# Kernel tuning notes

Hardware: AMD Instinct MI355X
Metric: run time of the kernel (lower is better)

Reference implementation:

```python
import jax, jax.numpy as jnp
import numpy as np

EMBED_DIM = 1024
WINDOW = 256
NUM_HEADS = 16
HEAD_DIM = EMBED_DIM // NUM_HEADS
SCALE = HEAD_DIM ** (-0.5)


def setup_inputs() -> dict:
    key = jax.random.key(0)
    ks = jax.random.split(key, 9)
    B, S, E = 4, 4096, EMBED_DIM
    std = E ** (-0.5)
    x = jax.random.normal(ks[0], (B, S, E), dtype=jnp.float32)
    Wq = jax.random.normal(ks[1], (E, E), dtype=jnp.float32) * std
    Wk = jax.random.normal(ks[2], (E, E), dtype=jnp.float32) * std
    Wv = jax.random.normal(ks[3], (E, E), dtype=jnp.float32) * std
    Wo = jax.random.normal(ks[4], (E, E), dtype=jnp.float32) * std
    bq = jax.random.normal(ks[5], (E,), dtype=jnp.float32) * 0.01
    bk = jax.random.normal(ks[6], (E,), dtype=jnp.float32) * 0.01
    bv = jax.random.normal(ks[7], (E,), dtype=jnp.float32) * 0.01
    bo = jax.random.normal(ks[8], (E,), dtype=jnp.float32) * 0.01
    return {"x": x, "Wq": Wq, "bq": bq, "Wk": Wk, "bk": bk,
            "Wv": Wv, "bv": bv, "Wo": Wo, "bo": bo}


def reference(x, Wq, bq, Wk, bk, Wv, bv, Wo, bo):
    B, S, E = x.shape
    W = WINDOW
    nw = S // W  # seq_len chosen divisible by window_size
    # projections (torch Linear: x @ W.T + b); no head split in the original
    q = x @ Wq.T + bq
    k = x @ Wk.T + bk
    v = x @ Wv.T + bv
    # split into non-overlapping windows: [B, nw, W, E]
    qw = q.reshape(B, nw, W, E)
    kw = k.reshape(B, nw, W, E)
    vw = v.reshape(B, nw, W, E)
    scores = jnp.einsum('bnqe,bnke->bnqk', qw, kw) * SCALE  # [B, nw, W, W]
    causal = jnp.tril(jnp.ones((W, W), dtype=bool))
    scores = jnp.where(causal, scores, -jnp.inf)
    attn = jax.nn.softmax(scores, axis=-1)
    out = jnp.einsum('bnqk,bnke->bnqe', attn, vw).reshape(B, S, E)
    out = out @ Wo.T + bo
    return out + x
```

## Files before the change

kernel.cpp:

```cpp
#include <hip/hip_runtime.h>
#include <hip/hip_bf16.h>


typedef unsigned short u16;
typedef __attribute__((ext_vector_type(8))) short short8;
typedef __attribute__((ext_vector_type(4))) float f32x4;

__device__ __forceinline__ u16 f2bf(float f) {
    __hip_bfloat16 h = __float2bfloat16(f);
    return __builtin_bit_cast(u16, h);
}

__global__ void cast_x(const float* __restrict__ x, u16* __restrict__ xb, u16* __restrict__ xt) {
    __shared__ float lt[64][65];
    const int t = threadIdx.x;
    const int e0 = blockIdx.x * 64, i0 = blockIdx.y * 64;
    const int tr = t >> 3, tc = (t & 7) * 8;
#pragma unroll
    for (int p = 0; p < 2; ++p) {
        int r = p * 32 + tr;
        const float* s = x + (size_t)(i0 + r) * 1024 + e0 + tc;
        float4 a = *(const float4*)s, b = *(const float4*)(s + 4);
        short8 o;
        o[0] = (short)f2bf(a.x); o[1] = (short)f2bf(a.y); o[2] = (short)f2bf(a.z); o[3] = (short)f2bf(a.w);
        o[4] = (short)f2bf(b.x); o[5] = (short)f2bf(b.y); o[6] = (short)f2bf(b.z); o[7] = (short)f2bf(b.w);
        *(short8*)(xb + (size_t)(i0 + r) * 1024 + e0 + tc) = o;
        lt[r][tc + 0] = a.x; lt[r][tc + 1] = a.y; lt[r][tc + 2] = a.z; lt[r][tc + 3] = a.w;
        lt[r][tc + 4] = b.x; lt[r][tc + 5] = b.y; lt[r][tc + 6] = b.z; lt[r][tc + 7] = b.w;
    }
    __syncthreads();
#pragma unroll
    for (int p = 0; p < 2; ++p) {
        int r = p * 32 + tr;
        short8 o;
#pragma unroll
        for (int j = 0; j < 8; ++j) o[j] = (short)f2bf(lt[tc + j][r]);
        *(short8*)(xt + (size_t)(e0 + r) * 16384 + i0 + tc) = o;
    }
}

__global__ void wcast(const float* __restrict__ Wq, const float* __restrict__ Wk,
                      const float* __restrict__ Wv, const float* __restrict__ Wo,
                      u16* __restrict__ WqT, u16* __restrict__ WkT,
                      u16* __restrict__ WvT, u16* __restrict__ Wob)
{
    __shared__ float lt[64][65];
    const int which = blockIdx.x >> 8;
    const int bid = blockIdx.x & 255;
    const int c0 = (bid & 15) * 64, r0 = (bid >> 4) * 64;
    const int t = threadIdx.x;
    const int tr = t >> 3, tc = (t & 7) * 8;
    const float* src = which == 0 ? Wq : which == 1 ? Wk : which == 2 ? Wv : Wo;
    if (which == 3) {
#pragma unroll
        for (int p = 0; p < 2; ++p) {
            int r = p * 32 + tr;
            const float* s = src + (size_t)(r0 + r) * 1024 + c0 + tc;
            float4 a = *(const float4*)s, b = *(const float4*)(s + 4);
            short8 o;
            o[0] = (short)f2bf(a.x); o[1] = (short)f2bf(a.y); o[2] = (short)f2bf(a.z); o[3] = (short)f2bf(a.w);
            o[4] = (short)f2bf(b.x); o[5] = (short)f2bf(b.y); o[6] = (short)f2bf(b.z); o[7] = (short)f2bf(b.w);
            *(short8*)(Wob + (size_t)(r0 + r) * 1024 + c0 + tc) = o;
        }
        return;
    }
    u16* dst = which == 0 ? WqT : which == 1 ? WkT : WvT;
#pragma unroll
    for (int p = 0; p < 2; ++p) {
        int r = p * 32 + tr;
        const float* s = src + (size_t)(r0 + r) * 1024 + c0 + tc;
        float4 a = *(const float4*)s, b = *(const float4*)(s + 4);
        lt[r][tc + 0] = a.x; lt[r][tc + 1] = a.y; lt[r][tc + 2] = a.z; lt[r][tc + 3] = a.w;
        lt[r][tc + 4] = b.x; lt[r][tc + 5] = b.y; lt[r][tc + 6] = b.z; lt[r][tc + 7] = b.w;
    }
    __syncthreads();
#pragma unroll
    for (int p = 0; p < 2; ++p) {
        int r = p * 32 + tr;
        short8 o;
#pragma unroll
        for (int j = 0; j < 8; ++j) o[j] = (short)f2bf(lt[tc + j][r]);
        *(short8*)(dst + (size_t)(c0 + r) * 1024 + r0 + tc) = o;
    }
}

__global__ void ub2(const float* __restrict__ Wk, const float* __restrict__ bq,
                    const float* __restrict__ Wo, const float* __restrict__ bv,
                    const float* __restrict__ bo, float* __restrict__ u, float* __restrict__ b2)
{
    const int t = threadIdx.x, bid = blockIdx.x;
    if (bid < 4) {
        int b = bid * 256 + t;
        float acc = 0.f;
        for (int o = 0; o < 1024; ++o) acc += Wk[(size_t)o * 1024 + b] * bq[o];
        u[b] = acc;
    } else {
        int n = (bid - 4) * 16 + (t >> 4);
        int l = t & 15;
        float acc = 0.f;
        for (int m = l; m < 1024; m += 16) acc += Wo[(size_t)n * 1024 + m] * bv[m];
#pragma unroll
        for (int s = 1; s < 16; s <<= 1) acc += __shfl_xor(acc, s, 64);
        if (l == 0) b2[n] = acc + bo[n];
    }
}

__global__ __launch_bounds__(256, 4) void gemm_small_dual(
    const u16* __restrict__ HA, const u16* __restrict__ HB, u16* __restrict__ HC,
    const u16* __restrict__ WA, const u16* __restrict__ WB, u16* __restrict__ WC)
{
    __shared__ __align__(16) u16 At[64 * 64], Bt[64 * 64];
    const bool sec = blockIdx.x >= 256;
    const u16* A = sec ? WA : HA;
    const u16* B = sec ? WB : HB;
    u16* C = sec ? WC : HC;
    const int bid = blockIdx.x & 255;
    const int m0 = (bid >> 4) * 64, n0 = (bid & 15) * 64;
    const int t = threadIdx.x, lane = t & 63, w = t >> 6;
    const int l15 = lane & 15, lk = lane >> 4;

    f32x4 acc[4];
#pragma unroll
    for (int m = 0; m < 4; ++m) acc[m] = (f32x4){0.f, 0.f, 0.f, 0.f};

    for (int k0 = 0; k0 < 1024; k0 += 64) {
        __syncthreads();
#pragma unroll
        for (int p = 0; p < 2; ++p) {
            int e = p * 2048 + t * 8;
            int row = e >> 6, col = e & 63;
            short8 va = *(const short8*)(A + (size_t)(m0 + row) * 1024 + k0 + col);
            *(short8*)((char*)At + row * 128 + ((col * 2) ^ ((row & 7) << 4))) = va;
            short8 vb = *(const short8*)(B + (size_t)(n0 + row) * 1024 + k0 + col);
            *(short8*)((char*)Bt + row * 128 + ((col * 2) ^ ((row & 7) << 4))) = vb;
        }
        __syncthreads();
#pragma unroll
        for (int ks = 0; ks < 2; ++ks) {
            int bc = ks * 64 + lk * 16;
            int brow = w * 16 + l15;
            short8 bfr = *(const short8*)((char*)Bt + brow * 128 + (bc ^ ((brow & 7) << 4)));
#pragma unroll
            for (int m = 0; m < 4; ++m) {
                int arow = m * 16 + l15;
                short8 af = *(const short8*)((char*)At + arow * 128 + (bc ^ ((arow & 7) << 4)));
                acc[m] = __builtin_amdgcn_mfma_f32_16x16x32_bf16(af, bfr, acc[m], 0, 0, 0);
            }
        }
    }
#pragma unroll
    for (int m = 0; m < 4; ++m)
#pragma unroll
        for (int r = 0; r < 4; ++r) {
            int row = m0 + m * 16 + lk * 4 + r;
            int col = n0 + w * 16 + l15;
            C[(size_t)row * 1024 + col] = f2bf(acc[m][r]);
        }
}

template <int EPI>
__global__ __launch_bounds__(256, 2) void gemm_bt(
    const u16* __restrict__ A, const u16* __restrict__ B,
    int M, int N, int K,
    const float* __restrict__ bias0,
    u16* __restrict__ Cb, float* __restrict__ Cf, const float* __restrict__ resid)
{
    __shared__ __align__(16) u16 At[128 * 64];
    __shared__ __align__(16) u16 Bt[128 * 64];
    const int t = threadIdx.x;
    const int lane = t & 63;
    const int wid = t >> 6;
    const int wm = wid >> 1, wn = wid & 1;
    const int l15 = lane & 15, lk = lane >> 4;

    const int bid = blockIdx.y * gridDim.x + blockIdx.x;
    const int nwg = gridDim.x * gridDim.y;
    const int cpx = nwg >> 3;
    const int swz = (bid & 7) * cpx + (bid >> 3);
    const int tn = swz & 7;
    const int tm = swz >> 3;
    const int m0 = tm * 128, n0 = tn * 128;

    const int srow = (t * 8) >> 6, scol = (t * 8) & 63;

    f32x4 acc[4][4];
#pragma unroll
    for (int m = 0; m < 4; ++m)
#pragma unroll
        for (int n = 0; n < 4; ++n)
            acc[m][n] = (f32x4){0.f, 0.f, 0.f, 0.f};

    short8 pva[4], pvb[4];
#pragma unroll
    for (int p = 0; p < 4; ++p) {
        pva[p] = *(const short8*)(A + (size_t)(m0 + p * 32 + srow) * K + scol);
        pvb[p] = *(const short8*)(B + (size_t)(n0 + p * 32 + srow) * K + scol);
    }

    for (int k0 = 0; k0 < K; k0 += 64) {
        __syncthreads();
#pragma unroll
        for (int p = 0; p < 4; ++p) {
            int row = p * 32 + srow;
            *(short8*)((char*)At + row * 128 + ((scol * 2) ^ ((row & 7) << 4))) = pva[p];
            *(short8*)((char*)Bt + row * 128 + ((scol * 2) ^ ((row & 7) << 4))) = pvb[p];
        }
        __syncthreads();
        if (k0 + 64 < K) {
#pragma unroll
            for (int p = 0; p < 4; ++p) {
                pva[p] = *(const short8*)(A + (size_t)(m0 + p * 32 + srow) * K + k0 + 64 + scol);
                pvb[p] = *(const short8*)(B + (size_t)(n0 + p * 32 + srow) * K + k0 + 64 + scol);
            }
        }
#pragma unroll
        for (int ks = 0; ks < 2; ++ks) {
            const int bc = ks * 64 + lk * 16;
            short8 af[4], bfr[4];
#pragma unroll
            for (int m = 0; m < 4; ++m) {
                int row = wm * 64 + m * 16 + l15;
                af[m] = *(const short8*)((char*)At + row * 128 + (bc ^ ((row & 7) << 4)));
            }
#pragma unroll
            for (int n = 0; n < 4; ++n) {
                int row = wn * 64 + n * 16 + l15;
                bfr[n] = *(const short8*)((char*)Bt + row * 128 + (bc ^ ((row & 7) << 4)));
            }
#pragma unroll
            for (int m = 0; m < 4; ++m)
#pragma unroll
                for (int n = 0; n < 4; ++n)
                    acc[m][n] = __builtin_amdgcn_mfma_f32_16x16x32_bf16(af[m], bfr[n], acc[m][n], 0, 0, 0);
        }
    }

#pragma unroll
    for (int m = 0; m < 4; ++m) {
#pragma unroll
        for (int n = 0; n < 4; ++n) {
            int col = n0 + wn * 64 + n * 16 + l15;
            float bv = bias0[col];
#pragma unroll
            for (int r = 0; r < 4; ++r) {
                int row = m0 + wm * 64 + m * 16 + lk * 4 + r;
                float v = acc[m][n][r] + bv;
                if (EPI == 0)
                    Cb[(size_t)row * N + col] = f2bf(v);
                else
                    Cf[(size_t)row * N + col] = v + resid[(size_t)row * N + col];
            }
        }
    }
}

__global__ __launch_bounds__(256, 2) void attn_win(
    const u16* __restrict__ y, const u16* __restrict__ xb,
    const u16* __restrict__ xt, u16* __restrict__ z)
{
    __shared__ __align__(16) char smem[75776];
    u16* Qt = (u16*)smem;
    u16* Kt = (u16*)(smem + 8192);
    u16* Vl = (u16*)smem;
    u16* P  = (u16*)(smem + 40960);
    float* rmax = (float*)(smem + 73728);
    float* rsum = (float*)(smem + 74752);

    const int t = threadIdx.x;
    const int lane = t & 63, wv = t >> 6;
    const int l15 = lane & 15, lk = lane >> 4;
    const int bid = blockIdx.x;
    const int swz = (bid & 7) * 32 + (bid >> 3);
    const int win = swz >> 2, qc = swz & 3;
    const size_t qrow0 = (size_t)win * 256 + qc * 64;
    const size_t krow0 = (size_t)win * 256;

    f32x4 acc[4][4];
#pragma unroll
    for (int m = 0; m < 4; ++m)
#pragma unroll
        for (int n = 0; n < 4; ++n)
            acc[m][n] = (f32x4){0.f, 0.f, 0.f, 0.f};

    for (int e0 = 0; e0 < 1024; e0 += 64) {
        __syncthreads();
#pragma unroll
        for (int p = 0; p < 2; ++p) {
            int e = p * 2048 + t * 8;
            int row = e >> 6, col = e & 63;
            short8 v = *(const short8*)(y + (qrow0 + row) * 1024 + e0 + col);
            *(short8*)((char*)Qt + row * 128 + ((col * 2) ^ ((row & 7) << 4))) = v;
        }
#pragma unroll
        for (int p = 0; p < 8; ++p) {
            int e = p * 2048 + t * 8;
            int row = e >> 6, col = e & 63;
            short8 v = *(const short8*)(xb + (krow0 + row) * 1024 + e0 + col);
            *(short8*)((char*)Kt + row * 128 + ((col * 2) ^ ((row & 7) << 4))) = v;
        }
        __syncthreads();
#pragma unroll
        for (int ks = 0; ks < 2; ++ks) {
            const int bc = ks * 64 + lk * 16;
            short8 af[4], bfr[4];
#pragma unroll
            for (int m = 0; m < 4; ++m) {
                int row = m * 16 + l15;
                af[m] = *(const short8*)((char*)Qt + row * 128 + (bc ^ ((row & 7) << 4)));
            }
#pragma unroll
            for (int n = 0; n < 4; ++n) {
                int row = wv * 64 + n * 16 + l15;
                bfr[n] = *(const short8*)((char*)Kt + row * 128 + (bc ^ ((row & 7) << 4)));
            }
            __builtin_amdgcn_s_setprio(1);
#pragma unroll
            for (int m = 0; m < 4; ++m)
#pragma unroll
                for (int n = 0; n < 4; ++n)
                    acc[m][n] = __builtin_amdgcn_mfma_f32_16x16x32_bf16(af[m], bfr[n], acc[m][n], 0, 0, 0);
            __builtin_amdgcn_s_setprio(0);
        }
    }

#pragma unroll
    for (int m = 0; m < 4; ++m)
#pragma unroll
        for (int n = 0; n < 4; ++n) {
            int col = wv * 64 + n * 16 + l15;
#pragma unroll
            for (int r = 0; r < 4; ++r) {
                int qpos = qc * 64 + m * 16 + lk * 4 + r;
                float v = acc[m][n][r] * 0.125f;
                acc[m][n][r] = (col <= qpos) ? v : -1e30f;
            }
        }
#pragma unroll
    for (int m = 0; m < 4; ++m)
#pragma unroll
        for (int r = 0; r < 4; ++r) {
            float tmx = fmaxf(fmaxf(acc[m][0][r], acc[m][1][r]), fmaxf(acc[m][2][r], acc[m][3][r]));
            tmx = fmaxf(tmx, __shfl_xor(tmx, 1));
            tmx = fmaxf(tmx, __shfl_xor(tmx, 2));
            tmx = fmaxf(tmx, __shfl_xor(tmx, 4));
            tmx = fmaxf(tmx, __shfl_xor(tmx, 8));
            if (l15 == 0) rmax[(m * 16 + lk * 4 + r) * 4 + wv] = tmx;
        }
    __syncthreads();
#pragma unroll
    for (int m = 0; m < 4; ++m)
#pragma unroll
        for (int r = 0; r < 4; ++r) {
            int row = m * 16 + lk * 4 + r;
            float m4 = fmaxf(fmaxf(rmax[row * 4], rmax[row * 4 + 1]),
                             fmaxf(rmax[row * 4 + 2], rmax[row * 4 + 3]));
            float s = 0.f;
#pragma unroll
            for (int n = 0; n < 4; ++n) {
                float e = __expf(acc[m][n][r] - m4);
                acc[m][n][r] = e;
                s += e;
            }
            s += __shfl_xor(s, 1);
            s += __shfl_xor(s, 2);
            s += __shfl_xor(s, 4);
            s += __shfl_xor(s, 8);
            if (l15 == 0) rsum[row * 4 + wv] = s;
        }
    __syncthreads();
#pragma unroll
    for (int m = 0; m < 4; ++m)
#pragma unroll
        for (int r = 0; r < 4; ++r) {
            int row = m * 16 + lk * 4 + r;
            float inv = 1.f / (rsum[row * 4] + rsum[row * 4 + 1] + rsum[row * 4 + 2] + rsum[row * 4 + 3]);
#pragma unroll
            for (int n = 0; n < 4; ++n) {
                int col = wv * 64 + n * 16 + l15;
                *(u16*)((char*)P + row * 512 + ((col * 2) ^ ((row & 7) << 4))) = f2bf(acc[m][n][r] * inv);
            }
        }

    for (int n0 = 0; n0 < 1024; n0 += 64) {
        __syncthreads();
#pragma unroll
        for (int p = 0; p < 8; ++p) {
            int e = p * 2048 + t * 8;
            int row = e >> 8, col = e & 255;
            short8 v = *(const short8*)(xt + (size_t)(n0 + row) * 16384 + win * 256 + col);
            *(short8*)((char*)Vl + row * 512 + ((col * 2) ^ ((row & 7) << 4))) = v;
        }
        __syncthreads();
        f32x4 acc2[4];
#pragma unroll
        for (int m = 0; m < 4; ++m) acc2[m] = (f32x4){0.f, 0.f, 0.f, 0.f};
#pragma unroll
        for (int ks = 0; ks < 8; ++ks) {
            const int bc = ks * 64 + lk * 16;
            short8 af[4];
#pragma unroll
            for (int m = 0; m < 4; ++m) {
                int row = m * 16 + l15;
                af[m] = *(const short8*)((char*)P + row * 512 + (bc ^ ((row & 7) << 4)));
            }
            int vrow = wv * 16 + l15;
            short8 bfr = *(const short8*)((char*)Vl + vrow * 512 + (bc ^ ((vrow & 7) << 4)));
            __builtin_amdgcn_s_setprio(1);
#pragma unroll
            for (int m = 0; m < 4; ++m)
                acc2[m] = __builtin_amdgcn_mfma_f32_16x16x32_bf16(af[m], bfr, acc2[m], 0, 0, 0);
            __builtin_amdgcn_s_setprio(0);
        }
#pragma unroll
        for (int m = 0; m < 4; ++m) {
#pragma unroll
            for (int r = 0; r < 4; ++r) {
                int row = m * 16 + lk * 4 + r;
                int col = n0 + wv * 16 + l15;
                z[(qrow0 + row) * 1024 + col] = f2bf(acc2[m][r]);
            }
        }
    }
}

extern "C" void kernel_launch(void* const* d_in, const int* in_sizes, int n_in,
                              void* d_out, int out_size, void* d_ws, size_t ws_size,
                              hipStream_t stream) {
    const float* x  = (const float*)d_in[0];
    const float* Wq = (const float*)d_in[1];
    const float* bq = (const float*)d_in[2];
    const float* Wk = (const float*)d_in[3];
    const float* Wv = (const float*)d_in[5];
    const float* bv = (const float*)d_in[6];
    const float* Wo = (const float*)d_in[7];
    const float* bo = (const float*)d_in[8];
    float* out = (float*)d_out;

    char* ws = (char*)d_ws;
    u16* xb  = (u16*)(ws);
    u16* xt  = (u16*)(ws + 33554432);
    u16* yb  = (u16*)(ws + 67108864);
    u16* zb  = (u16*)(ws + 100663296);
    u16* WqT = (u16*)(ws + 134217728);
    u16* WkT = (u16*)(ws + 136314880);
    u16* WvT = (u16*)(ws + 138412032);
    u16* Wob = (u16*)(ws + 140509184);
    u16* Hb  = (u16*)(ws + 142606336);
    u16* W2b = (u16*)(ws + 144703488);
    float* u_  = (float*)(ws + 146800640);
    float* b2_ = (float*)(ws + 146804736);

    cast_x<<<dim3(16, 256), 256, 0, stream>>>(x, xb, xt);
    wcast<<<1024, 256, 0, stream>>>(Wq, Wk, Wv, Wo, WqT, WkT, WvT, Wob);
    ub2<<<68, 256, 0, stream>>>(Wk, bq, Wo, bv, bo, u_, b2_);
    gemm_small_dual<<<512, 256, 0, stream>>>(WkT, WqT, Hb, Wob, WvT, W2b);
    gemm_bt<0><<<dim3(8, 128), 256, 0, stream>>>(xb, Hb, 16384, 1024, 1024, u_, yb, nullptr, nullptr);
    attn_win<<<256, 256, 0, stream>>>(yb, xb, xt, zb);
    gemm_bt<1><<<dim3(8, 128), 256, 0, stream>>>(zb, W2b, 16384, 1024, 1024, b2_, nullptr, out, x);
}
```

Measured before the change: 223.4 us.

## Widen GEMM blocks to 8 waves and halve attention query tile

```diff
diff --git a/kernel.cpp b/kernel.cpp
--- a/kernel.cpp
+++ b/kernel.cpp
@@ -159,7 +159,7 @@
 }
 
 template <int EPI>
-__global__ __launch_bounds__(256, 2) void gemm_bt(
+__global__ __launch_bounds__(512, 4) void gemm_bt(
     const u16* __restrict__ A, const u16* __restrict__ B,
     int M, int N, int K,
     const float* __restrict__ bias0,
@@ -169,8 +169,8 @@
     __shared__ __align__(16) u16 Bt[128 * 64];
     const int t = threadIdx.x;
     const int lane = t & 63;
-    const int wid = t >> 6;
-    const int wm = wid >> 1, wn = wid & 1;
+    const int w = t >> 6;
+    const int wm = w >> 2, wn = w & 3;
     const int l15 = lane & 15, lk = lane >> 4;
 
     const int bid = blockIdx.y * gridDim.x + blockIdx.x;
@@ -181,70 +181,58 @@
     const int tm = swz >> 3;
     const int m0 = tm * 128, n0 = tn * 128;
 
-    const int srow = (t * 8) >> 6, scol = (t * 8) & 63;
-
-    f32x4 acc[4][4];
-#pragma unroll
-    for (int m = 0; m < 4; ++m)
-#pragma unroll
-        for (int n = 0; n < 4; ++n)
-            acc[m][n] = (f32x4){0.f, 0.f, 0.f, 0.f};
-
-    short8 pva[4], pvb[4];
-#pragma unroll
-    for (int p = 0; p < 4; ++p) {
-        pva[p] = *(const short8*)(A + (size_t)(m0 + p * 32 + srow) * K + scol);
-        pvb[p] = *(const short8*)(B + (size_t)(n0 + p * 32 + srow) * K + scol);
-    }
+    const int srow = t >> 3, scol = (t & 7) * 8;
+
+    f32x4 acc[4][2];
+#pragma unroll
+    for (int mf = 0; mf < 4; ++mf)
+#pragma unroll
+        for (int nf = 0; nf < 2; ++nf)
+            acc[mf][nf] = (f32x4){0.f, 0.f, 0.f, 0.f};
 
     for (int k0 = 0; k0 < K; k0 += 64) {
         __syncthreads();
 #pragma unroll
-        for (int p = 0; p < 4; ++p) {
-            int row = p * 32 + srow;
-            *(short8*)((char*)At + row * 128 + ((scol * 2) ^ ((row & 7) << 4))) = pva[p];
-            *(short8*)((char*)Bt + row * 128 + ((scol * 2) ^ ((row & 7) << 4))) = pvb[p];
-        }
-        __syncthreads();
-        if (k0 + 64 < K) {
-#pragma unroll
-            for (int p = 0; p < 4; ++p) {
-                pva[p] = *(const short8*)(A + (size_t)(m0 + p * 32 + srow) * K + k0 + 64 + scol);
-                pvb[p] = *(const short8*)(B + (size_t)(n0 + p * 32 + srow) * K + k0 + 64 + scol);
-            }
-        }
+        for (int p = 0; p < 2; ++p) {
+            int row = p * 64 + srow;
+            short8 va = *(const short8*)(A + (size_t)(m0 + row) * K + k0 + scol);
+            *(short8*)((char*)At + row * 128 + ((scol * 2) ^ ((row & 7) << 4))) = va;
+            short8 vb = *(const short8*)(B + (size_t)(n0 + row) * K + k0 + scol);
+            *(short8*)((char*)Bt + row * 128 + ((scol * 2) ^ ((row & 7) << 4))) = vb;
+        }
+        __syncthreads();
 #pragma unroll
         for (int ks = 0; ks < 2; ++ks) {
             const int bc = ks * 64 + lk * 16;
-            short8 af[4], bfr[4];
-#pragma unroll
-            for (int m = 0; m < 4; ++m) {
-                int row = wm * 64 + m * 16 + l15;
-                af[m] = *(const short8*)((char*)At + row * 128 + (bc ^ ((row & 7) << 4)));
-            }
-#pragma unroll
-            for (int n = 0; n < 4; ++n) {
-                int row = wn * 64 + n * 16 + l15;
-                bfr[n] = *(const short8*)((char*)Bt + row * 128 + (bc ^ ((row & 7) << 4)));
-            }
-#pragma unroll
-            for (int m = 0; m < 4; ++m)
-#pragma unroll
-                for (int n = 0; n < 4; ++n)
-                    acc[m][n] = __builtin_amdgcn_mfma_f32_16x16x32_bf16(af[m], bfr[n], acc[m][n], 0, 0, 0);
-        }
-    }
-
-#pragma unroll
-    for (int m = 0; m < 4; ++m) {
-#pragma unroll
-        for (int n = 0; n < 4; ++n) {
-            int col = n0 + wn * 64 + n * 16 + l15;
+            short8 af[4], bfr[2];
+#pragma unroll
+            for (int mf = 0; mf < 4; ++mf) {
+                int row = wm * 64 + mf * 16 + l15;
+                af[mf] = *(const short8*)((char*)At + row * 128 + (bc ^ ((row & 7) << 4)));
+            }
+#pragma unroll
+            for (int nf = 0; nf < 2; ++nf) {
+                int row = wn * 32 + nf * 16 + l15;
+                bfr[nf] = *(const short8*)((char*)Bt + row * 128 + (bc ^ ((row & 7) << 4)));
+            }
+#pragma unroll
+            for (int mf = 0; mf < 4; ++mf)
+#pragma unroll
+                for (int nf = 0; nf < 2; ++nf)
+                    acc[mf][nf] = __builtin_amdgcn_mfma_f32_16x16x32_bf16(af[mf], bfr[nf], acc[mf][nf], 0, 0, 0);
+        }
+    }
+
+#pragma unroll
+    for (int mf = 0; mf < 4; ++mf) {
+#pragma unroll
+        for (int nf = 0; nf < 2; ++nf) {
+            int col = n0 + wn * 32 + nf * 16 + l15;
             float bv = bias0[col];
 #pragma unroll
             for (int r = 0; r < 4; ++r) {
-                int row = m0 + wm * 64 + m * 16 + lk * 4 + r;
-                float v = acc[m][n][r] + bv;
+                int row = m0 + wm * 64 + mf * 16 + lk * 4 + r;
+                float v = acc[mf][nf][r] + bv;
                 if (EPI == 0)
                     Cb[(size_t)row * N + col] = f2bf(v);
                 else
@@ -258,36 +246,34 @@
     const u16* __restrict__ y, const u16* __restrict__ xb,
     const u16* __restrict__ xt, u16* __restrict__ z)
 {
-    __shared__ __align__(16) char smem[75776];
+    __shared__ __align__(16) char smem[54272];
     u16* Qt = (u16*)smem;
-    u16* Kt = (u16*)(smem + 8192);
+    u16* Kt = (u16*)(smem + 4096);
     u16* Vl = (u16*)smem;
-    u16* P  = (u16*)(smem + 40960);
-    float* rmax = (float*)(smem + 73728);
-    float* rsum = (float*)(smem + 74752);
+    u16* P  = (u16*)(smem + 36864);
+    float* rmax = (float*)(smem + 53248);
+    float* rsum = (float*)(smem + 53760);
 
     const int t = threadIdx.x;
     const int lane = t & 63, wv = t >> 6;
     const int l15 = lane & 15, lk = lane >> 4;
     const int bid = blockIdx.x;
-    const int swz = (bid & 7) * 32 + (bid >> 3);
-    const int win = swz >> 2, qc = swz & 3;
-    const size_t qrow0 = (size_t)win * 256 + qc * 64;
+    const int swz = (bid & 7) * 64 + (bid >> 3);
+    const int win = swz >> 3, qc = swz & 7;
+    const size_t qrow0 = (size_t)win * 256 + qc * 32;
     const size_t krow0 = (size_t)win * 256;
 
-    f32x4 acc[4][4];
-#pragma unroll
-    for (int m = 0; m < 4; ++m)
+    f32x4 acc[2][4];
+#pragma unroll
+    for (int m = 0; m < 2; ++m)
 #pragma unroll
         for (int n = 0; n < 4; ++n)
             acc[m][n] = (f32x4){0.f, 0.f, 0.f, 0.f};
 
     for (int e0 = 0; e0 < 1024; e0 += 64) {
         __syncthreads();
-#pragma unroll
-        for (int p = 0; p < 2; ++p) {
-            int e = p * 2048 + t * 8;
-            int row = e >> 6, col = e & 63;
+        {
+            int row = t >> 3, col = (t & 7) * 8;
             short8 v = *(const short8*)(y + (qrow0 + row) * 1024 + e0 + col);
             *(short8*)((char*)Qt + row * 128 + ((col * 2) ^ ((row & 7) << 4))) = v;
         }
@@ -302,9 +288,9 @@
 #pragma unroll
         for (int ks = 0; ks < 2; ++ks) {
             const int bc = ks * 64 + lk * 16;
-            short8 af[4], bfr[4];
-#pragma unroll
-            for (int m = 0; m < 4; ++m) {
+            short8 af[2], bfr[4];
+#pragma unroll
+            for (int m = 0; m < 2; ++m) {
                 int row = m * 16 + l15;
                 af[m] = *(const short8*)((char*)Qt + row * 128 + (bc ^ ((row & 7) << 4)));
             }
@@ -315,7 +301,7 @@
             }
             __builtin_amdgcn_s_setprio(1);
 #pragma unroll
-            for (int m = 0; m < 4; ++m)
+            for (int m = 0; m < 2; ++m)
 #pragma unroll
                 for (int n = 0; n < 4; ++n)
                     acc[m][n] = __builtin_amdgcn_mfma_f32_16x16x32_bf16(af[m], bfr[n], acc[m][n], 0, 0, 0);
@@ -324,19 +310,19 @@
     }
 
 #pragma unroll
-    for (int m = 0; m < 4; ++m)
+    for (int m = 0; m < 2; ++m)
 #pragma unroll
         for (int n = 0; n < 4; ++n) {
             int col = wv * 64 + n * 16 + l15;
 #pragma unroll
             for (int r = 0; r < 4; ++r) {
-                int qpos = qc * 64 + m * 16 + lk * 4 + r;
+                int qpos = qc * 32 + m * 16 + lk * 4 + r;
                 float v = acc[m][n][r] * 0.125f;
                 acc[m][n][r] = (col <= qpos) ? v : -1e30f;
             }
         }
 #pragma unroll
-    for (int m = 0; m < 4; ++m)
+    for (int m = 0; m < 2; ++m)
 #pragma unroll
         for (int r = 0; r < 4; ++r) {
             float tmx = fmaxf(fmaxf(acc[m][0][r], acc[m][1][r]), fmaxf(acc[m][2][r], acc[m][3][r]));
@@ -348,7 +334,7 @@
         }
     __syncthreads();
 #pragma unroll
-    for (int m = 0; m < 4; ++m)
+    for (int m = 0; m < 2; ++m)
 #pragma unroll
         for (int r = 0; r < 4; ++r) {
             int row = m * 16 + lk * 4 + r;
@@ -369,7 +355,7 @@
         }
     __syncthreads();
 #pragma unroll
-    for (int m = 0; m < 4; ++m)
+    for (int m = 0; m < 2; ++m)
 #pragma unroll
         for (int r = 0; r < 4; ++r) {
             int row = m * 16 + lk * 4 + r;
@@ -391,15 +377,15 @@
             *(short8*)((char*)Vl + row * 512 + ((col * 2) ^ ((row & 7) << 4))) = v;
         }
         __syncthreads();
-        f32x4 acc2[4];
-#pragma unroll
-        for (int m = 0; m < 4; ++m) acc2[m] = (f32x4){0.f, 0.f, 0.f, 0.f};
+        f32x4 acc2[2];
+#pragma unroll
+        for (int m = 0; m < 2; ++m) acc2[m] = (f32x4){0.f, 0.f, 0.f, 0.f};
 #pragma unroll
         for (int ks = 0; ks < 8; ++ks) {
             const int bc = ks * 64 + lk * 16;
-            short8 af[4];
-#pragma unroll
-            for (int m = 0; m < 4; ++m) {
+            short8 af[2];
+#pragma unroll
+            for (int m = 0; m < 2; ++m) {
                 int row = m * 16 + l15;
                 af[m] = *(const short8*)((char*)P + row * 512 + (bc ^ ((row & 7) << 4)));
             }
@@ -407,12 +393,12 @@
             short8 bfr = *(const short8*)((char*)Vl + vrow * 512 + (bc ^ ((vrow & 7) << 4)));
             __builtin_amdgcn_s_setprio(1);
 #pragma unroll
-            for (int m = 0; m < 4; ++m)
+            for (int m = 0; m < 2; ++m)
                 acc2[m] = __builtin_amdgcn_mfma_f32_16x16x32_bf16(af[m], bfr, acc2[m], 0, 0, 0);
             __builtin_amdgcn_s_setprio(0);
         }
 #pragma unroll
-        for (int m = 0; m < 4; ++m) {
+        for (int m = 0; m < 2; ++m) {
 #pragma unroll
             for (int r = 0; r < 4; ++r) {
                 int row = m * 16 + lk * 4 + r;
@@ -454,7 +440,7 @@
     wcast<<<1024, 256, 0, stream>>>(Wq, Wk, Wv, Wo, WqT, WkT, WvT, Wob);
     ub2<<<68, 256, 0, stream>>>(Wk, bq, Wo, bv, bo, u_, b2_);
     gemm_small_dual<<<512, 256, 0, stream>>>(WkT, WqT, Hb, Wob, WvT, W2b);
-    gemm_bt<0><<<dim3(8, 128), 256, 0, stream>>>(xb, Hb, 16384, 1024, 1024, u_, yb, nullptr, nullptr);
-    attn_win<<<256, 256, 0, stream>>>(yb, xb, xt, zb);
-    gemm_bt<1><<<dim3(8, 128), 256, 0, stream>>>(zb, W2b, 16384, 1024, 1024, b2_, nullptr, out, x);
-}
+    gemm_bt<0><<<dim3(8, 128), 512, 0, stream>>>(xb, Hb, 16384, 1024, 1024, u_, yb, nullptr, nullptr);
+    attn_win<<<512, 256, 0, stream>>>(yb, xb, xt, zb);
+    gemm_bt<1><<<dim3(8, 128), 512, 0, stream>>>(zb, W2b, 16384, 1024, 1024, b2_, nullptr, out, x);
+}
```

Result: no change. 226.0 us (+1.1%).
